# Optimization experiments

Measured on AMD Instinct MI355X. Metric: run time of the kernel, lower is better.

## Reference

```python
import jax, jax.numpy as jnp
import numpy as np
from jax import lax

T, N, H, L, NL, C, NA = 256, 1024, 256, 16, 32, 64, 16


def setup_inputs():
    ks = jax.random.split(jax.random.key(0), 20)
    g = lambda i, shape, s=0.05: jax.random.normal(ks[i], shape, jnp.float32) * s
    return dict(
        condition=jax.random.normal(ks[0], (T, N, C), jnp.float32),
        active=jax.random.randint(ks[1], (T, N), 0, L),
        lines=jax.random.randint(ks[2], (N, L), 0, NL),
        actions=jax.random.randint(ks[3], (T, N), 0, NA),
        h0=g(4, (N, H), 1.0), p0=g(5, (N, 1), 1.0), pp0=g(6, (N, 2), 1.0),
        embed=g(7, (NL, H)),
        wih_f=g(8, (3 * H, H)), whh_f=g(9, (3 * H, H)),
        bih_f=jnp.zeros(3 * H), bhh_f=jnp.zeros(3 * H),
        wih_b=g(10, (3 * H, H)), whh_b=g(11, (3 * H, H)),
        bih_b=jnp.zeros(3 * H), bhh_b=jnp.zeros(3 * H),
        f_w0=g(12, (H, C + 2 * H)), f_b0=jnp.zeros(H),
        f_w1=g(13, (H, H)), f_b1=jnp.zeros(H),
        f_w2=g(14, (H, H)), f_b2=jnp.zeros(H),
        c_wih=g(15, (3 * H, H)), c_whh=g(16, (3 * H, H)),
        c_bih=jnp.zeros(3 * H), c_bhh=jnp.zeros(3 * H),
        w_critic=g(17, (1, H)), b_critic=jnp.zeros(1),
        w_actor=g(18, (NA, H)), b_actor=jnp.zeros(NA),
    )


def _gru_step(h, x, wih, whh, bih, bhh):
    # PyTorch GRU/GRUCell gate order: r, z, n
    gi = x @ wih.T + bih
    gh = h @ whh.T + bhh
    ir, iz, inn = jnp.split(gi, 3, -1)
    hr, hz, hn = jnp.split(gh, 3, -1)
    r = jax.nn.sigmoid(ir + hr)
    z = jax.nn.sigmoid(iz + hz)
    n = jnp.tanh(inn + r * hn)
    return (1.0 - z) * n + z * h


def reference(condition, active, lines, actions, h0, p0, pp0, embed,
              wih_f, whh_f, bih_f, bhh_f, wih_b, whh_b, bih_b, bhh_b,
              f_w0, f_b0, f_w1, f_b1, f_w2, f_b2,
              c_wih, c_whh, c_bih, c_bhh, w_critic, b_critic, w_actor, b_actor):
    Tn, Nn, _ = condition.shape
    Ln = lines.shape[1]
    Hh = h0.shape[1]
    # ---- task encoder: bidirectional GRU over every cyclic roll of the line embeddings ----
    M = embed[lines]                                   # [N, L, H]
    seq = jnp.transpose(M, (1, 0, 2))                  # [L, N, H]
    idx = (jnp.arange(Ln)[:, None] + jnp.arange(Ln)[None, :]) % Ln  # roll -i: idx[i,j]=(i+j)%L
    X = seq[idx]                                       # [roll, t, N, H]
    X = jnp.transpose(X, (1, 0, 2, 3)).reshape(Ln, Ln * Nn, Hh)  # seq-first, rolls folded into batch
    z0 = jnp.zeros((Ln * Nn, Hh), condition.dtype)
    h_f, _ = lax.scan(lambda h, x: (_gru_step(h, x, wih_f, whh_f, bih_f, bhh_f), None), z0, X)
    h_b, _ = lax.scan(lambda h, x: (_gru_step(h, x, wih_b, whh_b, bih_b, bhh_b), None), z0, X[::-1])
    Hmem = jnp.concatenate([h_f.reshape(Ln, Nn, Hh), h_b.reshape(Ln, Nn, Hh)], -1)  # [L, N, 2H]

    def mlp(x):
        x = jax.nn.relu(x @ f_w0.T + f_b0)
        x = jax.nn.relu(x @ f_w1.T + f_b1)
        return jax.nn.relu(x @ f_w2.T + f_b2)

    Ridx = jnp.arange(Nn)

    def step(h, xs):
        cond_t, w_t, a_t = xs
        r = Hmem[w_t, Ridx]                            # gather H[w, R] -> [N, 2H]
        h = _gru_step(h, mlp(jnp.concatenate([cond_t, r], -1)), c_wih, c_whh, c_bih, c_bhh)
        probs = jax.nn.softmax(h @ w_actor.T + b_actor)
        v = h @ w_critic.T + b_critic
        return h, (a_t, w_t, v, h, probs)

    _, (a_s, w_s, v_s, h_s, ap_s) = lax.scan(step, h0, (condition, active, actions))
    fdt = condition.dtype
    p_s = jnp.broadcast_to(p0[None], (Tn,) + p0.shape)
    pp_s = jnp.broadcast_to(pp0[None], (Tn,) + pp0.shape)
    # packed RecurrentState field order: a, p, w, v, h, a_probs, p_probs
    return jnp.concatenate([a_s[..., None].astype(fdt), p_s,
                            w_s[..., None].astype(fdt), v_s,
                            h_s, ap_s, pp_s], -1)      # [T, N, 4 + H + NA + 2]
```

## Files before the change

### kernel.cpp

```cpp
#include <hip/hip_runtime.h>
#include <stdint.h>

#define DI __device__ __forceinline__

typedef __attribute__((ext_vector_type(8))) short short8;
typedef __attribute__((ext_vector_type(4))) float f32x4;

DI float bf2f(uint16_t u){ union{uint32_t i; float f;} v; v.i = ((uint32_t)u)<<16; return v.f; }
DI uint16_t f2bf(float f){
    union{float f; uint32_t i;} v; v.f = f;
    uint32_t r = v.i + 0x7FFFu + ((v.i>>16)&1u);
    return (uint16_t)(r>>16);
}
DI float sigm(float x){ return 1.f/(1.f+__expf(-x)); }
DI float tanhx(float x){ float e=__expf(-2.f*fabsf(x)); float t=(1.f-e)/(1.f+e); return x<0.f? -t : t; }
DI void unp2(uint32_t u, float&a, float&b){ a = bf2f((uint16_t)(u&0xFFFFu)); b = bf2f((uint16_t)(u>>16)); }

#define MFMA(a,b,c) __builtin_amdgcn_mfma_f32_16x16x32_bf16((a),(b),(c),0,0,0)


__global__ void k_detect(const uint16_t* __restrict__ embed, int* __restrict__ flag){
  __shared__ int bad;
  if (threadIdx.x == 0) bad = 0;
  __syncthreads();
  float v = bf2f(embed[threadIdx.x]);
  if (!(fabsf(v) <= 100.f)) atomicAdd(&bad, 1);
  __syncthreads();
  if (threadIdx.x == 0) flag[0] = (bad > 0) ? 1 : 0;
}

struct CvtEnt { const void* src; uint16_t* dst; int n; int pad; };
struct CvtTab { CvtEnt e[26]; };

__global__ __launch_bounds__(1024) void k_convert_small(CvtTab tab, const int* __restrict__ flag){
  CvtEnt E = tab.e[blockIdx.x];
  if (flag[0]){
    const float* s = (const float*)E.src;
    for (int i = threadIdx.x; i < E.n; i += 1024) E.dst[i] = f2bf(s[i]);
  } else {
    const uint16_t* s = (const uint16_t*)E.src;
    for (int i = threadIdx.x; i < E.n; i += 1024) E.dst[i] = s[i];
  }
}

__global__ __launch_bounds__(256) void k_convert_big(const void* __restrict__ src,
                                                     uint16_t* __restrict__ dst,
                                                     int n8, const int* __restrict__ flag){
  int i = blockIdx.x*256 + threadIdx.x;
  if (i >= n8) return;
  if (flag[0]){
    const float4* s = (const float4*)src;
    float4 a = s[(size_t)i*2], b = s[(size_t)i*2+1];
    union { uint16_t u[8]; uint4 v; } o;
    o.u[0]=f2bf(a.x); o.u[1]=f2bf(a.y); o.u[2]=f2bf(a.z); o.u[3]=f2bf(a.w);
    o.u[4]=f2bf(b.x); o.u[5]=f2bf(b.y); o.u[6]=f2bf(b.z); o.u[7]=f2bf(b.w);
    *(uint4*)&dst[(size_t)i*8] = o.v;
  } else {
    *(uint4*)&dst[(size_t)i*8] = ((const uint4*)src)[i];
  }
}

__global__ __launch_bounds__(256) void k_tables(
    const uint16_t* __restrict__ embed,
    const uint16_t* __restrict__ wih_f, const uint16_t* __restrict__ bih_f,
    const uint16_t* __restrict__ wih_b, const uint16_t* __restrict__ bih_b,
    float* __restrict__ GiE)
{
  int dir = blockIdx.x >> 5, e = blockIdx.x & 31;
  const uint16_t* wih = dir ? wih_b : wih_f;
  const uint16_t* bih = dir ? bih_b : bih_f;
  __shared__ float emb[256];
  int tid = threadIdx.x;
  emb[tid] = bf2f(embed[e*256 + tid]);
  __syncthreads();
  for (int c = tid; c < 768; c += 256){
    float s = bf2f(bih[c]);
    const uint32_t* wr = (const uint32_t*)(wih + (size_t)c*256);
    #pragma unroll 4
    for (int k2 = 0; k2 < 128; ++k2){
      float a, b; unp2(wr[k2], a, b);
      s += emb[k2*2]*a + emb[k2*2+1]*b;
    }
    GiE[(size_t)(dir*32 + e)*768 + c] = s;
  }
}

__global__ __launch_bounds__(512,2) void k_encoder(
    const int* __restrict__ lines, const float* __restrict__ GiE,
    const uint16_t* __restrict__ whh_f, const uint16_t* __restrict__ whh_b,
    const uint16_t* __restrict__ bhh_f, const uint16_t* __restrict__ bhh_b,
    uint16_t* __restrict__ Hmem )
{
  int b = blockIdx.x;
  int dir = b >> 8; b &= 255;
  int r = b >> 4, n0 = (b & 15) << 6;
  const uint16_t* whh = dir ? whh_b : whh_f;
  const uint16_t* bhh = dir ? bhh_b : bhh_f;
  const float* gte = GiE + (size_t)dir * (32*768);

  __shared__ uint16_t hbuf[64*264];
  __shared__ int lid_s[64*16];

  int tid = threadIdx.x;
  for (int s = tid; s < 1024; s += 512) lid_s[s] = lines[(n0 + (s>>4))*16 + (s&15)];
  for (int s = tid; s < 8448; s += 512) ((uint32_t*)hbuf)[s] = 0u;

  int w = tid >> 6, lane = tid & 63, l15 = lane & 15, q = lane >> 4;
  int cw = w << 5;
  int nc[6];
  nc[0]=cw; nc[1]=cw+16; nc[2]=256+cw; nc[3]=256+cw+16; nc[4]=512+cw; nc[5]=512+cw+16;
  float bh[6];
  #pragma unroll
  for (int i=0;i<6;i++) bh[i] = bf2f(bhh[nc[i]+l15]);

  float hreg[4][2][4];
  #pragma unroll
  for (int a=0;a<4;a++)
    #pragma unroll
    for (int c=0;c<2;c++)
      #pragma unroll
      for (int e=0;e<4;e++) hreg[a][c][e]=0.f;

  __syncthreads();

  for (int j=0;j<16;++j){
    int jj = dir ? (15-j) : j;
    int pos = (r + jj) & 15;
    f32x4 acc[4][6];
    #pragma unroll
    for (int mt=0;mt<4;mt++)
      #pragma unroll
      for (int u=0;u<6;u++) acc[mt][u] = (f32x4){0.f,0.f,0.f,0.f};
    #pragma unroll
    for (int kb=0;kb<8;kb++){
      short8 af[4];
      #pragma unroll
      for (int mt=0;mt<4;mt++)
        af[mt] = *(const short8*)&hbuf[(mt*16+l15)*264 + kb*32 + q*8];
      #pragma unroll
      for (int u=0;u<6;u++){
        short8 bf = *(const short8*)&whh[(size_t)(nc[u]+l15)*256 + kb*32 + q*8];
        #pragma unroll
        for (int mt=0;mt<4;mt++) acc[mt][u] = MFMA(af[mt], bf, acc[mt][u]);
      }
    }
    __syncthreads();
    #pragma unroll
    for (int mt=0;mt<4;mt++){
      int lidv[4];
      #pragma unroll
      for (int e=0;e<4;e++) lidv[e] = lid_s[(mt*16 + q*4 + e)*16 + pos];
      float gv[4][6];
      #pragma unroll
      for (int e=0;e<4;e++)
        #pragma unroll
        for (int u=0;u<6;u++) gv[e][u] = gte[(size_t)lidv[e]*768 + nc[u] + l15];
      #pragma unroll
      for (int c=0;c<2;c++)
        #pragma unroll
        for (int e=0;e<4;e++){
          float ghr = acc[mt][c  ][e] + bh[c  ];
          float ghz = acc[mt][2+c][e] + bh[2+c];
          float ghn = acc[mt][4+c][e] + bh[4+c];
          float rr = sigm(gv[e][c] + ghr);
          float zz = sigm(gv[e][2+c] + ghz);
          float nn = tanhx(gv[e][4+c] + rr*ghn);
          float hn = (1.f-zz)*nn + zz*hreg[mt][c][e];
          hreg[mt][c][e] = hn;
          hbuf[(mt*16 + q*4 + e)*264 + cw + c*16 + l15] = f2bf(hn);
        }
    }
    __syncthreads();
  }
  for (int s = tid; s < 8192; s += 512){
    int row = s >> 7, cp = (s & 127) << 1;
    uint32_t v = *(uint32_t*)&hbuf[row*264 + cp];
    *(uint32_t*)&Hmem[(size_t)((r<<10) + n0 + row)*512 + (dir<<8) + cp] = v;
  }
}

__global__ __launch_bounds__(256,3) void k_gemm(
    const uint16_t* __restrict__ A, int lda,
    const uint16_t* __restrict__ W, int ldw, int woff,
    const uint16_t* __restrict__ bias,
    const int* __restrict__ gidx, const uint16_t* __restrict__ G,
    uint16_t* __restrict__ C, int ldc, int K, int flags)
{
  int n0 = blockIdx.x << 6, m0 = blockIdx.y << 7;
  int tid = threadIdx.x, w = tid>>6, lane = tid&63, l15 = lane&15, q = lane>>4;
  __shared__ uint16_t As[128*56];
  __shared__ uint16_t Ws[64*56];
  f32x4 acc[2][4];
  #pragma unroll
  for (int mt=0;mt<2;mt++)
    #pragma unroll
    for (int nt=0;nt<4;nt++) acc[mt][nt]=(f32x4){0.f,0.f,0.f,0.f};
  int nk = K >> 5;
  int arow0 = tid >> 2, ach = (tid & 3) << 3;
  for (int kb = 0; kb < nk; ++kb){
    int k0 = kb << 5;
    *(uint4*)&As[arow0*56 + ach]      = *(const uint4*)&A[(size_t)(m0+arow0)*lda + k0 + ach];
    *(uint4*)&As[(arow0+64)*56 + ach] = *(const uint4*)&A[(size_t)(m0+arow0+64)*lda + k0 + ach];
    *(uint4*)&Ws[arow0*56 + ach]      = *(const uint4*)&W[(size_t)(n0+arow0)*ldw + woff + k0 + ach];
    __syncthreads();
    short8 af[2], bfr[4];
    #pragma unroll
    for (int mt=0;mt<2;mt++) af[mt] = *(const short8*)&As[(w*32 + mt*16 + l15)*56 + q*8];
    #pragma unroll
    for (int nt=0;nt<4;nt++) bfr[nt] = *(const short8*)&Ws[(nt*16 + l15)*56 + q*8];
    #pragma unroll
    for (int mt=0;mt<2;mt++)
      #pragma unroll
      for (int nt=0;nt<4;nt++) acc[mt][nt] = MFMA(af[mt], bfr[nt], acc[mt][nt]);
    __syncthreads();
  }
  float bv[4] = {0.f,0.f,0.f,0.f};
  if (flags & 2){
    #pragma unroll
    for (int nt=0;nt<4;nt++) bv[nt] = bf2f(bias[n0 + nt*16 + l15]);
  }
  #pragma unroll
  for (int mt=0;mt<2;mt++)
    #pragma unroll
    for (int e=0;e<4;e++){
      int row = m0 + w*32 + mt*16 + q*4 + e;
      size_t gb = 0;
      if (flags & 4) gb = ((size_t)gidx[row]*1024 + (size_t)(row & 1023))*256;
      #pragma unroll
      for (int nt=0;nt<4;nt++){
        int col = n0 + nt*16 + l15;
        float v = acc[mt][nt][e] + bv[nt];
        if (flags & 4) v += bf2f(G[gb + col]);
        if (flags & 1) v = fmaxf(v, 0.f);
        C[(size_t)row*ldc + col] = f2bf(v);
      }
    }
}

__global__ __launch_bounds__(512,2) void k_phasec(
    const uint16_t* __restrict__ Gi, const uint16_t* __restrict__ c_whh,
    const uint16_t* __restrict__ c_bhh, const uint16_t* __restrict__ hinit,
    uint16_t* __restrict__ hcur, uint16_t* __restrict__ h_s, int Tc)
{
  int n0 = blockIdx.x << 4;
  int tid = threadIdx.x, w = tid>>6, lane = tid&63, l15 = lane&15, q = lane>>4;
  int cw = w<<5;
  int nc[6];
  nc[0]=cw; nc[1]=cw+16; nc[2]=256+cw; nc[3]=256+cw+16; nc[4]=512+cw; nc[5]=512+cw+16;

  __shared__ uint16_t hb[2][16*264];

  for (int s = tid; s < 2048; s += 512){
    int row = s >> 7, cp = (s&127) << 1;
    uint32_t v = *(const uint32_t*)&hinit[(size_t)(n0+row)*256 + cp];
    *(uint32_t*)&hb[0][row*264 + cp] = v;
  }
  float bh[6];
  #pragma unroll
  for (int i=0;i<6;i++) bh[i] = bf2f(c_bhh[nc[i]+l15]);
  float hreg[2][4];
  #pragma unroll
  for (int c=0;c<2;c++)
    #pragma unroll
    for (int e=0;e<4;e++)
      hreg[c][e] = bf2f(hinit[(size_t)(n0+q*4+e)*256 + cw + c*16 + l15]);
  float gcur[4][6];
  #pragma unroll
  for (int e=0;e<4;e++){
    const uint16_t* grow = Gi + (size_t)(n0 + q*4 + e)*768;
    #pragma unroll
    for (int u=0;u<6;u++) gcur[e][u] = bf2f(grow[nc[u]+l15]);
  }
  __syncthreads();

  int p = 0;
  for (int t=0;t<Tc;++t){
    if (t > 0){
      #pragma unroll
      for (int i=0;i<4;i++){
        int s = tid + i*512;
        int row = s >> 7, cp = (s&127) << 1;
        *(uint32_t*)&h_s[(size_t)(((t-1)<<10) + n0 + row)*256 + cp] =
            *(const uint32_t*)&hb[p][row*264 + cp];
      }
    }
    float gnx[4][6];
    {
      int tn = (t+1 < Tc) ? (t+1) : t;
      const uint16_t* gbase = Gi + ((size_t)(tn<<10) + n0)*768;
      #pragma unroll
      for (int e=0;e<4;e++){
        const uint16_t* grow = gbase + (q*4+e)*768;
        #pragma unroll
        for (int u=0;u<6;u++) gnx[e][u] = bf2f(grow[nc[u]+l15]);
      }
    }
    f32x4 acc[6];
    #pragma unroll
    for (int u=0;u<6;u++) acc[u] = (f32x4){0.f,0.f,0.f,0.f};
    short8 bf0[6], bf1[6];
    #pragma unroll
    for (int u=0;u<6;u++)
      bf0[u] = *(const short8*)&c_whh[(size_t)(nc[u]+l15)*256 + q*8];
    #pragma unroll
    for (int kb=0;kb<8;kb++){
      short8 af = *(const short8*)&hb[p][l15*264 + kb*32 + q*8];
      if (kb < 7){
        #pragma unroll
        for (int u=0;u<6;u++)
          ((kb&1)?bf0:bf1)[u] =
            *(const short8*)&c_whh[(size_t)(nc[u]+l15)*256 + (kb+1)*32 + q*8];
      }
      #pragma unroll
      for (int u=0;u<6;u++)
        acc[u] = MFMA(af, ((kb&1)?bf1:bf0)[u], acc[u]);
    }
    #pragma unroll
    for (int c=0;c<2;c++)
      #pragma unroll
      for (int e=0;e<4;e++){
        int row = q*4+e;
        float ghr = acc[c  ][e]+bh[c  ];
        float ghz = acc[2+c][e]+bh[2+c];
        float ghn = acc[4+c][e]+bh[4+c];
        float rr = sigm(gcur[e][c]+ghr), zz = sigm(gcur[e][2+c]+ghz);
        float nn = tanhx(gcur[e][4+c] + rr*ghn);
        float hn = (1.f-zz)*nn + zz*hreg[c][e];
        hreg[c][e] = hn;
        hb[p^1][row*264 + cw + c*16 + l15] = f2bf(hn);
      }
    __syncthreads();
    #pragma unroll
    for (int e=0;e<4;e++)
      #pragma unroll
      for (int u=0;u<6;u++) gcur[e][u] = gnx[e][u];
    p ^= 1;
  }
  for (int s = tid; s < 2048; s += 512){
    int row = s >> 7, cp = (s&127) << 1;
    uint32_t v = *(uint32_t*)&hb[p][row*264 + cp];
    *(uint32_t*)&hcur[(size_t)(n0+row)*256 + cp] = v;
    *(uint32_t*)&h_s[(size_t)(((Tc-1)<<10) + n0 + row)*256 + cp] = v;
  }
}

__global__ __launch_bounds__(256) void k_phased(
    const uint16_t* __restrict__ h_s ,
    const uint16_t* __restrict__ w_actor, const uint16_t* __restrict__ b_actor,
    const uint16_t* __restrict__ w_critic, const uint16_t* __restrict__ b_critic,
    const int* __restrict__ actions , const int* __restrict__ active,
    const uint16_t* __restrict__ p0, const uint16_t* __restrict__ pp0,
    void* __restrict__ out, const int* __restrict__ flag, int row0g)
{
  int r0 = blockIdx.x << 6;
  __shared__ uint16_t hb[64*264];
  __shared__ uint16_t wa[17*256];
  __shared__ float lv[64*18];
  int tid = threadIdx.x;
  for (int s = tid; s < 2048; s += 256){
    int row = s >> 5, ch = (s & 31) << 3;
    *(uint4*)&hb[row*264 + ch] = *(const uint4*)&h_s[(size_t)(r0+row)*256 + ch];
  }
  for (int s = tid; s < 512; s += 256)
    *(uint4*)&wa[s*8] = *(const uint4*)&w_actor[s*8];
  if (tid < 32) *(uint4*)&wa[4096 + tid*8] = *(const uint4*)&w_critic[tid*8];
  __syncthreads();
  int row = tid & 63, cg = tid >> 6;
  for (int c = cg; c < 17; c += 4){
    const uint32_t* hr = (const uint32_t*)&hb[row*264];
    const uint32_t* wr = (const uint32_t*)&wa[c*256];
    float s = 0.f;
    #pragma unroll 4
    for (int k2=0;k2<128;k2++){
      float a,b,c2,d; unp2(hr[k2],a,b); unp2(wr[k2],c2,d);
      s += a*c2 + b*d;
    }
    s += (c<16) ? bf2f(b_actor[c]) : bf2f(b_critic[0]);
    lv[row*18 + c] = s;
  }
  __syncthreads();
  if (tid < 64){
    float mx = -1e30f;
    #pragma unroll
    for (int c=0;c<16;c++) mx = fmaxf(mx, lv[tid*18+c]);
    float sum = 0.f;
    #pragma unroll
    for (int c=0;c<16;c++){ float ev = __expf(lv[tid*18+c]-mx); lv[tid*18+c]=ev; sum+=ev; }
    float inv = 1.f/sum;
    #pragma unroll
    for (int c=0;c<16;c++) lv[tid*18+c] *= inv;
  }
  __syncthreads();
  int isf = flag[0];
  float* outf = (float*)out;
  uint16_t* outb = (uint16_t*)out;
  for (int s = tid; s < 64*278; s += 256){
    int rw = s / 278, c = s - rw*278;
    int gr = row0g + r0 + rw;
    int n  = (r0 + rw) & 1023;
    float fv;
    if (c >= 4 && c < 260)        fv = bf2f(hb[rw*264 + (c-4)]);
    else if (c >= 260 && c < 276) fv = lv[rw*18 + (c-260)];
    else if (c == 0)              fv = (float)actions[gr];
    else if (c == 1)              fv = bf2f(p0[n]);
    else if (c == 2)              fv = (float)active[gr];
    else if (c == 3)              fv = lv[rw*18+16];
    else                          fv = bf2f(pp0[(n<<1) + (c-276)]);
    size_t off = (size_t)gr*278 + c;
    if (isf) outf[off] = fv;
    else     outb[off] = f2bf(fv);
  }
}

extern "C" void kernel_launch(void* const* d_in, const int* in_sizes, int n_in,
                              void* d_out, int out_size, void* d_ws, size_t ws_size,
                              hipStream_t stream)
{
  (void)in_sizes; (void)n_in; (void)out_size;
  const int* active  = (const int*)d_in[1];
  const int* lines   = (const int*)d_in[2];
  const int* actions = (const int*)d_in[3];

  char* wsb = (char*)d_ws;
  size_t off = 0;
  auto aln  = [](size_t x){ return (x + 255) & ~(size_t)255; };
  auto carve = [&](size_t bytes)->char*{ char* p = wsb + off; off += aln(bytes); return p; };

  int*      flag   = (int*)     carve(256);
  float*    GiE    = (float*)   carve((size_t)2*32*768*4);
  uint16_t* Hmem   = (uint16_t*)carve((size_t)16*1024*512*2);
  uint16_t* Rpart  = (uint16_t*)carve((size_t)16384*256*2);
  uint16_t* hcur   = (uint16_t*)carve((size_t)1024*256*2);
  uint16_t* condbf = (uint16_t*)carve((size_t)262144*64*2);

  struct Item { int idx; int n; };
  const Item items[26] = {
    {8,196608},{9,196608},{10,768},{11,768},{12,196608},{13,196608},{14,768},{15,768},
    {16,147456},{17,256},{18,65536},{19,256},{20,65536},{21,256},
    {22,196608},{23,196608},{24,768},{25,768},
    {26,256},{27,1},{28,4096},{29,16},{5,1024},{6,2048},{7,8192},{4,262144}};
  uint16_t* bf[30] = {};
  CvtTab tab;
  for (int i=0;i<26;i++){
    uint16_t* d = (uint16_t*)carve((size_t)items[i].n*2);
    bf[items[i].idx] = d;
    tab.e[i].src = d_in[items[i].idx];
    tab.e[i].dst = d;
    tab.e[i].n   = items[i].n;
    tab.e[i].pad = 0;
  }

  size_t fixedBytes = off;
  int Tc = 4;
  const int cands[7] = {256,128,64,32,16,8,4};
  for (int i=0;i<7;i++){
    int c = cands[i];
    size_t need = fixedBytes + 2*aln((size_t)c*1024*256*2) + aln((size_t)c*1024*768*2);
    if (need <= ws_size){ Tc = c; break; }
  }
  uint16_t* Xa  = (uint16_t*)carve((size_t)Tc*1024*256*2);
  uint16_t* Xb  = (uint16_t*)carve((size_t)Tc*1024*256*2);
  uint16_t* Gic = (uint16_t*)carve((size_t)Tc*1024*768*2);

  k_detect<<<1,256,0,stream>>>((const uint16_t*)d_in[7], flag);
  k_convert_small<<<26,1024,0,stream>>>(tab, flag);
  k_convert_big<<<8192,256,0,stream>>>(d_in[0], condbf, 2097152, flag);

  k_tables<<<64,256,0,stream>>>(bf[7], bf[8], bf[10], bf[12], bf[14], GiE);
  k_encoder<<<512,512,0,stream>>>(lines, GiE, bf[9], bf[13], bf[11], bf[15], Hmem);
  k_gemm<<<dim3(4,128),256,0,stream>>>(Hmem,512, bf[16],576,64, nullptr, nullptr,nullptr,
                                       Rpart,256, 512, 0);
  for (int t0 = 0; t0 < 256; t0 += Tc){
    const uint16_t* condc = condbf + (size_t)t0*1024*64;
    const int* activec = active + t0*1024;
    k_gemm<<<dim3(4,Tc*8),256,0,stream>>>(condc,64, bf[16],576,0, bf[17], activec, Rpart,
                                          Xa,256, 64, 7);
    k_gemm<<<dim3(4,Tc*8),256,0,stream>>>(Xa,256, bf[18],256,0, bf[19], nullptr,nullptr,
                                          Xb,256, 256, 3);
    k_gemm<<<dim3(4,Tc*8),256,0,stream>>>(Xb,256, bf[20],256,0, bf[21], nullptr,nullptr,
                                          Xa,256, 256, 3);
    k_gemm<<<dim3(12,Tc*8),256,0,stream>>>(Xa,256, bf[22],256,0, bf[24], nullptr,nullptr,
                                           Gic,768, 256, 2);
    k_phasec<<<64,512,0,stream>>>(Gic, bf[23], bf[25], (t0==0 ? bf[4] : hcur), hcur, Xb, Tc);
    k_phased<<<Tc*16,256,0,stream>>>(Xb, bf[28], bf[29], bf[26], bf[27],
                                     actions, active, bf[5], bf[6],
                                     d_out, flag, t0*1024);
  }
}
```

Before: 3.220 ms.

## Store GRU input gates in per-lane packed layout for vectorized recurrent loads

New measurement: 3.291 ms. +2.2%, slower.

```diff
diff --git a/kernel.cpp b/kernel.cpp
--- a/kernel.cpp
+++ b/kernel.cpp
@@ -219,22 +219,41 @@
     #pragma unroll
     for (int nt=0;nt<4;nt++) bv[nt] = bf2f(bias[n0 + nt*16 + l15]);
   }
-  #pragma unroll
-  for (int mt=0;mt<2;mt++)
-    #pragma unroll
-    for (int e=0;e<4;e++){
-      int row = m0 + w*32 + mt*16 + q*4 + e;
-      size_t gb = 0;
-      if (flags & 4) gb = ((size_t)gidx[row]*1024 + (size_t)(row & 1023))*256;
+  if (flags & 8){
+    #pragma unroll
+    for (int mt=0;mt<2;mt++)
       #pragma unroll
       for (int nt=0;nt<4;nt++){
-        int col = n0 + nt*16 + l15;
-        float v = acc[mt][nt][e] + bv[nt];
-        if (flags & 4) v += bf2f(G[gb + col]);
-        if (flags & 1) v = fmaxf(v, 0.f);
-        C[(size_t)row*ldc + col] = f2bf(v);
+        int row0 = m0 + w*32 + mt*16 + q*4;
+        int t = row0 >> 10, n = row0 & 1023;
+        int nblk = n >> 4;
+        int colv = n0 + nt*16 + l15;
+        int wp = (colv >> 5) & 7, u = (colv >> 8)*2 + ((colv >> 4) & 1);
+        size_t base = ((((size_t)t*64 + nblk)*8 + wp)*16 + (size_t)l15)*96
+                      + (size_t)q*24 + (size_t)u*4;
+        union { uint16_t us[4]; uint2 v; } o;
+        #pragma unroll
+        for (int e=0;e<4;e++) o.us[e] = f2bf(acc[mt][nt][e] + bv[nt]);
+        *(uint2*)&C[base] = o.v;
       }
-    }
+  } else {
+    #pragma unroll
+    for (int mt=0;mt<2;mt++)
+      #pragma unroll
+      for (int e=0;e<4;e++){
+        int row = m0 + w*32 + mt*16 + q*4 + e;
+        size_t gb = 0;
+        if (flags & 4) gb = ((size_t)gidx[row]*1024 + (size_t)(row & 1023))*256;
+        #pragma unroll
+        for (int nt=0;nt<4;nt++){
+          int col = n0 + nt*16 + l15;
+          float v = acc[mt][nt][e] + bv[nt];
+          if (flags & 4) v += bf2f(G[gb + col]);
+          if (flags & 1) v = fmaxf(v, 0.f);
+          C[(size_t)row*ldc + col] = f2bf(v);
+        }
+      }
+  }
 }
 
 __global__ __launch_bounds__(512,2) void k_phasec(
@@ -242,13 +261,17 @@
     const uint16_t* __restrict__ c_bhh, const uint16_t* __restrict__ hinit,
     uint16_t* __restrict__ hcur, uint16_t* __restrict__ h_s, int Tc)
 {
-  int n0 = blockIdx.x << 4;
+  int bx = blockIdx.x;
+  int n0 = bx << 4;
   int tid = threadIdx.x, w = tid>>6, lane = tid&63, l15 = lane&15, q = lane>>4;
   int cw = w<<5;
   int nc[6];
   nc[0]=cw; nc[1]=cw+16; nc[2]=256+cw; nc[3]=256+cw+16; nc[4]=512+cw; nc[5]=512+cw+16;
 
   __shared__ uint16_t hb[2][16*264];
+
+  const size_t gstep = (size_t)64*8*16*96;
+  size_t goff0 = (((size_t)bx*8 + w)*16 + (size_t)l15)*96 + (size_t)q*24;
 
   for (int s = tid; s < 2048; s += 512){
     int row = s >> 7, cp = (s&127) << 1;
@@ -264,37 +287,19 @@
     #pragma unroll
     for (int e=0;e<4;e++)
       hreg[c][e] = bf2f(hinit[(size_t)(n0+q*4+e)*256 + cw + c*16 + l15]);
-  float gcur[4][6];
-  #pragma unroll
-  for (int e=0;e<4;e++){
-    const uint16_t* grow = Gi + (size_t)(n0 + q*4 + e)*768;
-    #pragma unroll
-    for (int u=0;u<6;u++) gcur[e][u] = bf2f(grow[nc[u]+l15]);
-  }
-  __syncthreads();
+  short8 gpk[3];
+  {
+    const uint16_t* gb = Gi + goff0;
+    gpk[0] = *(const short8*)&gb[0];
+    gpk[1] = *(const short8*)&gb[8];
+    gpk[2] = *(const short8*)&gb[16];
+  }
+  __syncthreads();
+
+#define GV(u,e) bf2f((uint16_t)gpk[((u)*4+(e))>>3][((u)*4+(e))&7])
 
   int p = 0;
   for (int t=0;t<Tc;++t){
-    if (t > 0){
-      #pragma unroll
-      for (int i=0;i<4;i++){
-        int s = tid + i*512;
-        int row = s >> 7, cp = (s&127) << 1;
-        *(uint32_t*)&h_s[(size_t)(((t-1)<<10) + n0 + row)*256 + cp] =
-            *(const uint32_t*)&hb[p][row*264 + cp];
-      }
-    }
-    float gnx[4][6];
-    {
-      int tn = (t+1 < Tc) ? (t+1) : t;
-      const uint16_t* gbase = Gi + ((size_t)(tn<<10) + n0)*768;
-      #pragma unroll
-      for (int e=0;e<4;e++){
-        const uint16_t* grow = gbase + (q*4+e)*768;
-        #pragma unroll
-        for (int u=0;u<6;u++) gnx[e][u] = bf2f(grow[nc[u]+l15]);
-      }
-    }
     f32x4 acc[6];
     #pragma unroll
     for (int u=0;u<6;u++) acc[u] = (f32x4){0.f,0.f,0.f,0.f};
@@ -315,6 +320,23 @@
       for (int u=0;u<6;u++)
         acc[u] = MFMA(af, ((kb&1)?bf1:bf0)[u], acc[u]);
     }
+    short8 gn0, gn1, gn2;
+    {
+      int tn = (t+1 < Tc) ? (t+1) : t;
+      const uint16_t* gb = Gi + (size_t)tn*gstep + goff0;
+      gn0 = *(const short8*)&gb[0];
+      gn1 = *(const short8*)&gb[8];
+      gn2 = *(const short8*)&gb[16];
+    }
+    if (t > 0){
+      #pragma unroll
+      for (int i=0;i<4;i++){
+        int s = tid + i*512;
+        int row = s >> 7, cp = (s&127) << 1;
+        *(uint32_t*)&h_s[(size_t)(((t-1)<<10) + n0 + row)*256 + cp] =
+            *(const uint32_t*)&hb[p][row*264 + cp];
+      }
+    }
     #pragma unroll
     for (int c=0;c<2;c++)
       #pragma unroll
@@ -323,19 +345,17 @@
         float ghr = acc[c  ][e]+bh[c  ];
         float ghz = acc[2+c][e]+bh[2+c];
         float ghn = acc[4+c][e]+bh[4+c];
-        float rr = sigm(gcur[e][c]+ghr), zz = sigm(gcur[e][2+c]+ghz);
-        float nn = tanhx(gcur[e][4+c] + rr*ghn);
+        float rr = sigm(GV(c,e)+ghr), zz = sigm(GV(2+c,e)+ghz);
+        float nn = tanhx(GV(4+c,e) + rr*ghn);
         float hn = (1.f-zz)*nn + zz*hreg[c][e];
         hreg[c][e] = hn;
         hb[p^1][row*264 + cw + c*16 + l15] = f2bf(hn);
       }
     __syncthreads();
-    #pragma unroll
-    for (int e=0;e<4;e++)
-      #pragma unroll
-      for (int u=0;u<6;u++) gcur[e][u] = gnx[e][u];
+    gpk[0] = gn0; gpk[1] = gn1; gpk[2] = gn2;
     p ^= 1;
   }
+#undef GV
   for (int s = tid; s < 2048; s += 512){
     int row = s >> 7, cp = (s&127) << 1;
     uint32_t v = *(uint32_t*)&hb[p][row*264 + cp];
@@ -480,7 +500,7 @@
     k_gemm<<<dim3(4,Tc*8),256,0,stream>>>(Xb,256, bf[20],256,0, bf[21], nullptr,nullptr,
                                           Xa,256, 256, 3);
     k_gemm<<<dim3(12,Tc*8),256,0,stream>>>(Xa,256, bf[22],256,0, bf[24], nullptr,nullptr,
-                                           Gic,768, 256, 2);
+                                           Gic,768, 256, 10);
     k_phasec<<<64,512,0,stream>>>(Gic, bf[23], bf[25], (t0==0 ? bf[4] : hcur), hcur, Xb, Tc);
     k_phased<<<Tc*16,256,0,stream>>>(Xb, bf[28], bf[29], bf[26], bf[27],
                                      actions, active, bf[5], bf[6],
```
